# Optimization experiments

Hardware: AMD Instinct MI355X
Metric: run time of the kernel (lower is better)

## Reference

```python
import jax, jax.numpy as jnp
import numpy as np
import math

T, B, D, H, L, C = 2048, 64, 256, 256, 2, 2
HIGHWAY_BIAS = 0.0
# SRU rescale factor for the highway skip term (rescale=True)
SCALE_X = (1.0 + math.exp(HIGHWAY_BIAS * 2)) ** 0.5


def setup_inputs() -> dict:
    key = jax.random.key(0)
    ks = jax.random.split(key, 8)
    s = 1.0 / np.sqrt(D)
    x = jax.random.normal(ks[0], (T, B, D), dtype=jnp.float32)
    # per-layer SRU weights: W [D, 3H] -> (x_tilde, f, r); bias [2H] -> (b_f, b_r)
    W1 = jax.random.uniform(ks[1], (D, 3 * H), jnp.float32, -s, s)
    b1 = jnp.zeros((2 * H,), jnp.float32)
    W2 = jax.random.uniform(ks[2], (H, 3 * H), jnp.float32, -s, s)
    b2 = jnp.zeros((2 * H,), jnp.float32)
    lin_W = jax.random.uniform(ks[3], (H, C), jnp.float32, -s, s)
    lin_b = jnp.zeros((C,), jnp.float32)
    return {"x": x, "W1": W1, "b1": b1, "W2": W2, "b2": b2,
            "lin_W": lin_W, "lin_b": lin_b}


def _sru_layer(x, W, b):
    # x: [T, B, D]; W: [D, 3H]; b: [2H]. Skip term uses raw x (D == H).
    U = jnp.einsum('tbd,dk->tbk', x, W)           # [T, B, 3H]
    x_tilde, f_raw, r_raw = jnp.split(U, 3, axis=-1)
    b_f, b_r = jnp.split(b, 2)
    f = jax.nn.sigmoid(f_raw + b_f + HIGHWAY_BIAS)  # [T, B, H]
    r = jax.nn.sigmoid(r_raw + b_r)                 # [T, B, H]

    def step(c, inp):
        f_t, xt_t = inp
        c = f_t * c + (1.0 - f_t) * xt_t
        return c, c

    c0 = jnp.zeros(x.shape[1:], x.dtype)            # [B, H]
    _, cs = jax.lax.scan(step, c0, (f, x_tilde))    # cs: [T, B, H]
    h = r * cs + (1.0 - r) * (x * SCALE_X)          # highway skip (rescaled)
    return h


def reference(x, W1, b1, W2, b2, lin_W, lin_b):
    h1 = _sru_layer(x, W1, b1)
    h2 = _sru_layer(h1, W2, b2)
    last = h2[-1]                                   # [B, H] (last timestep)
    # Dropout in eval mode = identity (deterministic reference)
    return last @ lin_W + lin_b                     # [B, C]
```

## Files before the change

kernel.cpp:

```cpp
#include <hip/hip_runtime.h>
#include <hip/hip_bf16.h>
#include <stdint.h>

#define T_LEN 2048
#define B_SZ  64
#define H_SZ  256
#define NH3   768
#define M_SZ  (T_LEN * B_SZ)
#define NC    64
#define TC    32
#define SCALE_X_F 1.41421356237309515f

typedef __attribute__((ext_vector_type(8))) short short8;
typedef __attribute__((ext_vector_type(4))) float f32x4;

__device__ __forceinline__ float sigmoidf_(float z) {
    return 1.0f / (1.0f + __expf(-z));
}
__device__ __forceinline__ unsigned short f2bf(float f) {
    unsigned u = __float_as_uint(f);
    return (unsigned short)((u + 0x7FFFu + ((u >> 16) & 1u)) >> 16);
}
__device__ __forceinline__ float bf2f(unsigned short s) {
    return __uint_as_float(((unsigned)s) << 16);
}

__global__ void k_convert_x(const float* __restrict__ x, unsigned short* __restrict__ xb) {
    int i = blockIdx.x * blockDim.x + threadIdx.x;
    const float4* in = (const float4*)x;
    float4 a = in[i * 2];
    float4 b = in[i * 2 + 1];
    short8 o;
    o[0] = (short)f2bf(a.x); o[1] = (short)f2bf(a.y);
    o[2] = (short)f2bf(a.z); o[3] = (short)f2bf(a.w);
    o[4] = (short)f2bf(b.x); o[5] = (short)f2bf(b.y);
    o[6] = (short)f2bf(b.z); o[7] = (short)f2bf(b.w);
    *(short8*)&xb[(size_t)i * 8] = o;
}

__global__ void k_prep_w(const float* __restrict__ W, unsigned short* __restrict__ Wt) {
    int i = blockIdx.x * 256 + threadIdx.x;
    int n = i >> 8, k = i & 255;
    Wt[i] = f2bf(W[(size_t)k * NH3 + n]);
}

template <int NT, int CS>
__global__ void k_gemm(const unsigned short* __restrict__ A,
                       const unsigned short* __restrict__ Bt,
                       unsigned short* __restrict__ C) {
    __shared__ alignas(16) unsigned short smem[128 * 128];
    unsigned short* As = smem;
    unsigned short* Bs = smem + 8192;

    const int cpx = (1024 * NT) / 8;
    int orig = blockIdx.x;
    int wgid = (orig & 7) * cpx + (orig >> 3);
    int mt = wgid / NT, nt = wgid % NT;
    int mbase = mt * 128, nbase = nt * 128;

    int tid = threadIdx.x;
    int w = tid >> 6, l = tid & 63;
    int r16 = l & 15, kg = l >> 4;
    int wr = w >> 1, wc = w & 1;
    int scol = ((l & 7) ^ (l >> 3)) * 8;
    int srow = (l >> 3);

    f32x4 acc[4][4];
    #pragma unroll
    for (int m = 0; m < 4; ++m)
        #pragma unroll
        for (int n = 0; n < 4; ++n) {
            f32x4 z = {0.f, 0.f, 0.f, 0.f};
            acc[m][n] = z;
        }

    for (int kt = 0; kt < 4; ++kt) {
        int k0 = kt * 64;
        #pragma unroll
        for (int p = 0; p < 4; ++p) {
            int row = w * 32 + p * 8 + srow;
            const unsigned short* ga = A  + (size_t)(mbase + row) * 256 + k0 + scol;
            const unsigned short* gb = Bt + (size_t)(nbase + row) * 256 + k0 + scol;
            __builtin_amdgcn_global_load_lds(
                (const __attribute__((address_space(1))) void*)ga,
                (__attribute__((address_space(3))) void*)&As[(w * 4 + p) * 512], 16, 0, 0);
            __builtin_amdgcn_global_load_lds(
                (const __attribute__((address_space(1))) void*)gb,
                (__attribute__((address_space(3))) void*)&Bs[(w * 4 + p) * 512], 16, 0, 0);
        }
        __syncthreads();

        short8 af[4][2], bfv[4][2];
        #pragma unroll
        for (int m = 0; m < 4; ++m) {
            int arow = wr * 64 + m * 16 + r16;
            int sw = (arow & 7) << 3;
            #pragma unroll
            for (int kk = 0; kk < 2; ++kk)
                af[m][kk] = *(const short8*)&As[arow * 64 + ((kk * 32 + kg * 8) ^ sw)];
        }
        #pragma unroll
        for (int n = 0; n < 4; ++n) {
            int brow = wc * 64 + n * 16 + r16;
            int sw = (brow & 7) << 3;
            #pragma unroll
            for (int kk = 0; kk < 2; ++kk)
                bfv[n][kk] = *(const short8*)&Bs[brow * 64 + ((kk * 32 + kg * 8) ^ sw)];
        }

        #pragma unroll
        for (int m = 0; m < 4; ++m)
            #pragma unroll
            for (int n = 0; n < 4; ++n)
                #pragma unroll
                for (int kk = 0; kk < 2; ++kk)
                    acc[m][n] = __builtin_amdgcn_mfma_f32_16x16x32_bf16(
                        af[m][kk], bfv[n][kk], acc[m][n], 0, 0, 0);
        __syncthreads();
    }

    #pragma unroll
    for (int m = 0; m < 4; ++m)
        #pragma unroll
        for (int n = 0; n < 4; ++n) {
            int col = wc * 64 + n * 16 + r16;
            #pragma unroll
            for (int r = 0; r < 4; ++r) {
                int row = wr * 64 + m * 16 + kg * 4 + r;
                smem[row * 128 + (col ^ ((row & 7) << 3))] = f2bf(acc[m][n][r]);
            }
        }
    __syncthreads();
    #pragma unroll
    for (int i = 0; i < 8; ++i) {
        int slot = i * 256 + tid;
        int row = slot >> 4, seg = slot & 15;
        short8 v = *(const short8*)&smem[row * 128 + ((seg * 8) ^ ((row & 7) << 3))];
        *(short8*)&C[(size_t)(mbase + row) * CS + nbase + seg * 8] = v;
    }
}

__global__ void k_passA(const unsigned short* __restrict__ U, const float* __restrict__ bias,
                        float* __restrict__ P, float* __restrict__ S, int stride) {
    int ci = blockIdx.x >> 6;
    int b  = blockIdx.x & 63;
    int h  = threadIdx.x;
    float bfv = bias[h];
    size_t base = ((size_t)(ci * TC) * B_SZ + b) * stride + h;
    float c = 0.f, pr = 1.f;
    #pragma unroll 4
    for (int t = 0; t < TC; ++t) {
        float xt = bf2f(U[base]);
        float fr = bf2f(U[base + 256]);
        float f = sigmoidf_(fr + bfv);
        c = f * c + (1.f - f) * xt;
        pr *= f;
        base += (size_t)B_SZ * stride;
    }
    int o = blockIdx.x * 256 + h;
    P[o] = pr;
    S[o] = c;
}

__global__ void k_passB(const float* __restrict__ P, const float* __restrict__ S,
                        float* __restrict__ cin) {
    int b = blockIdx.x, h = threadIdx.x;
    int idx = b * 256 + h;
    float c = 0.f;
    #pragma unroll 8
    for (int ci = 0; ci < NC; ++ci) {
        cin[ci * 16384 + idx] = c;
        c = P[ci * 16384 + idx] * c + S[ci * 16384 + idx];
    }
    cin[NC * 16384 + idx] = c;
}

__global__ void k_passC(const unsigned short* __restrict__ U, const float* __restrict__ bias,
                        const unsigned short* __restrict__ xb, const float* __restrict__ cin,
                        unsigned short* __restrict__ hout) {
    int ci = blockIdx.x >> 6, b = blockIdx.x & 63, h = threadIdx.x;
    float bfv = bias[h], brv = bias[256 + h];
    float c = cin[blockIdx.x * 256 + h];
    size_t base  = ((size_t)(ci * TC) * B_SZ + b) * NH3 + h;
    size_t xbase = ((size_t)(ci * TC) * B_SZ + b) * H_SZ + h;
    #pragma unroll 4
    for (int t = 0; t < TC; ++t) {
        float xt = bf2f(U[base]);
        float fr = bf2f(U[base + 256]);
        float rr = bf2f(U[base + 512]);
        float f = sigmoidf_(fr + bfv);
        float r = sigmoidf_(rr + brv);
        c = f * c + (1.f - f) * xt;
        float xv = bf2f(xb[xbase]);
        hout[xbase] = f2bf(r * c + (1.f - r) * xv * SCALE_X_F);
        base  += (size_t)B_SZ * NH3;
        xbase += (size_t)B_SZ * H_SZ;
    }
}

__global__ void k_final(const unsigned short* __restrict__ h1, const float* __restrict__ cin,
                        const float* __restrict__ W2, const float* __restrict__ b2,
                        const float* __restrict__ lw, const float* __restrict__ lb,
                        float* __restrict__ out) {
    int b = blockIdx.x, h = threadIdx.x;
    __shared__ float hrow[256];
    size_t hb = ((size_t)(T_LEN - 1) * B_SZ + b) * H_SZ;
    hrow[h] = bf2f(h1[hb + h]);
    __syncthreads();
    float rr = 0.f;
    #pragma unroll 8
    for (int k = 0; k < 256; ++k)
        rr += hrow[k] * W2[(size_t)k * NH3 + 512 + h];
    float r = sigmoidf_(rr + b2[256 + h]);
    float c = cin[NC * 16384 + b * 256 + h];
    float hv = r * c + (1.f - r) * hrow[h] * SCALE_X_F;
    float p0 = hv * lw[h * 2];
    float p1 = hv * lw[h * 2 + 1];
    #pragma unroll
    for (int off = 32; off; off >>= 1) {
        p0 += __shfl_down(p0, off);
        p1 += __shfl_down(p1, off);
    }
    __shared__ float s0[4], s1[4];
    int wid = h >> 6, lane = h & 63;
    if (lane == 0) { s0[wid] = p0; s1[wid] = p1; }
    __syncthreads();
    if (h == 0) {
        out[b * 2]     = s0[0] + s0[1] + s0[2] + s0[3] + lb[0];
        out[b * 2 + 1] = s1[0] + s1[1] + s1[2] + s1[3] + lb[1];
    }
}

extern "C" void kernel_launch(void* const* d_in, const int* in_sizes, int n_in,
                              void* d_out, int out_size, void* d_ws, size_t ws_size,
                              hipStream_t stream) {
    const float* x   = (const float*)d_in[0];
    const float* W1  = (const float*)d_in[1];
    const float* b1  = (const float*)d_in[2];
    const float* W2  = (const float*)d_in[3];
    const float* b2  = (const float*)d_in[4];
    const float* lw  = (const float*)d_in[5];
    const float* lb  = (const float*)d_in[6];
    float* out = (float*)d_out;

    char* ws = (char*)d_ws;
    unsigned short* U   = (unsigned short*)ws;
    unsigned short* xb  = (unsigned short*)(ws + 201326592);
    unsigned short* h1  = (unsigned short*)(ws + 268435456);
    unsigned short* Wt1 = (unsigned short*)(ws + 335544320);
    unsigned short* Wt2 = (unsigned short*)(ws + 335937536);
    float* Pbuf = (float*)(ws + 336330752);
    float* Sbuf = (float*)(ws + 340525056);
    float* cin  = (float*)(ws + 344719360);

    k_convert_x<<<16384, 256, 0, stream>>>(x, xb);
    k_prep_w<<<768, 256, 0, stream>>>(W1, Wt1);
    k_prep_w<<<512, 256, 0, stream>>>(W2, Wt2);

    k_gemm<6, NH3><<<6144, 256, 0, stream>>>(xb, Wt1, U);
    k_passA<<<4096, 256, 0, stream>>>(U, b1, Pbuf, Sbuf, NH3);
    k_passB<<<64, 256, 0, stream>>>(Pbuf, Sbuf, cin);
    k_passC<<<4096, 256, 0, stream>>>(U, b1, xb, cin, h1);

    k_gemm<4, 512><<<4096, 256, 0, stream>>>(h1, Wt2, U);
    k_passA<<<4096, 256, 0, stream>>>(U, b2, Pbuf, Sbuf, 512);
    k_passB<<<64, 256, 0, stream>>>(Pbuf, Sbuf, cin);
    k_final<<<64, 256, 0, stream>>>(h1, cin, W2, b2, lw, lb, out);
}
```

Baseline: 413.6 us.

## Double-buffer LDS tiles in bf16 GEMM to overlap loads with MFMA

The projection GEMM now keeps two LDS buffers each for the A and B tiles. It issues the global-to-LDS loads for the next K-slice before running the MFMAs on the current one, and drops one barrier per iteration. The goal is to hide global memory latency behind matrix compute. In exchange, LDS use per block doubles and a launch bound of 2 blocks per CU is added, which may reduce occupancy.

```diff
diff --git a/kernel.cpp b/kernel.cpp
--- a/kernel.cpp
+++ b/kernel.cpp
@@ -45,12 +45,12 @@
 }
 
 template <int NT, int CS>
-__global__ void k_gemm(const unsigned short* __restrict__ A,
-                       const unsigned short* __restrict__ Bt,
-                       unsigned short* __restrict__ C) {
-    __shared__ alignas(16) unsigned short smem[128 * 128];
-    unsigned short* As = smem;
-    unsigned short* Bs = smem + 8192;
+__global__ void __launch_bounds__(256, 2)
+k_gemm(const unsigned short* __restrict__ A,
+       const unsigned short* __restrict__ Bt,
+       unsigned short* __restrict__ C) {
+    __shared__ alignas(16) unsigned short As[2][8192];
+    __shared__ alignas(16) unsigned short Bs[2][8192];
 
     const int cpx = (1024 * NT) / 8;
     int orig = blockIdx.x;
@@ -65,6 +65,22 @@
     int scol = ((l & 7) ^ (l >> 3)) * 8;
     int srow = (l >> 3);
 
+    const unsigned short* aBase = A  + (size_t)(mbase + w * 32 + srow) * 256 + scol;
+    const unsigned short* bBase = Bt + (size_t)(nbase + w * 32 + srow) * 256 + scol;
+
+    #define STAGE(buf, kt)                                                        \
+        do {                                                                      \
+            _Pragma("unroll")                                                     \
+            for (int p = 0; p < 4; ++p) {                                         \
+                __builtin_amdgcn_global_load_lds(                                 \
+                    (const __attribute__((address_space(1))) void*)(aBase + (size_t)p * 8 * 256 + (kt) * 64), \
+                    (__attribute__((address_space(3))) void*)&As[buf][(w * 4 + p) * 512], 16, 0, 0); \
+                __builtin_amdgcn_global_load_lds(                                 \
+                    (const __attribute__((address_space(1))) void*)(bBase + (size_t)p * 8 * 256 + (kt) * 64), \
+                    (__attribute__((address_space(3))) void*)&Bs[buf][(w * 4 + p) * 512], 16, 0, 0); \
+            }                                                                     \
+        } while (0)
+
     f32x4 acc[4][4];
     #pragma unroll
     for (int m = 0; m < 4; ++m)
@@ -74,21 +90,13 @@
             acc[m][n] = z;
         }
 
+    STAGE(0, 0);
+    __syncthreads();
+
+    int cur = 0;
+    #pragma unroll
     for (int kt = 0; kt < 4; ++kt) {
-        int k0 = kt * 64;
-        #pragma unroll
-        for (int p = 0; p < 4; ++p) {
-            int row = w * 32 + p * 8 + srow;
-            const unsigned short* ga = A  + (size_t)(mbase + row) * 256 + k0 + scol;
-            const unsigned short* gb = Bt + (size_t)(nbase + row) * 256 + k0 + scol;
-            __builtin_amdgcn_global_load_lds(
-                (const __attribute__((address_space(1))) void*)ga,
-                (__attribute__((address_space(3))) void*)&As[(w * 4 + p) * 512], 16, 0, 0);
-            __builtin_amdgcn_global_load_lds(
-                (const __attribute__((address_space(1))) void*)gb,
-                (__attribute__((address_space(3))) void*)&Bs[(w * 4 + p) * 512], 16, 0, 0);
-        }
-        __syncthreads();
+        if (kt < 3) STAGE(cur ^ 1, kt + 1);
 
         short8 af[4][2], bfv[4][2];
         #pragma unroll
@@ -97,7 +105,7 @@
             int sw = (arow & 7) << 3;
             #pragma unroll
             for (int kk = 0; kk < 2; ++kk)
-                af[m][kk] = *(const short8*)&As[arow * 64 + ((kk * 32 + kg * 8) ^ sw)];
+                af[m][kk] = *(const short8*)&As[cur][arow * 64 + ((kk * 32 + kg * 8) ^ sw)];
         }
         #pragma unroll
         for (int n = 0; n < 4; ++n) {
@@ -105,7 +113,7 @@
             int sw = (brow & 7) << 3;
             #pragma unroll
             for (int kk = 0; kk < 2; ++kk)
-                bfv[n][kk] = *(const short8*)&Bs[brow * 64 + ((kk * 32 + kg * 8) ^ sw)];
+                bfv[n][kk] = *(const short8*)&Bs[cur][brow * 64 + ((kk * 32 + kg * 8) ^ sw)];
         }
 
         #pragma unroll
@@ -116,9 +124,13 @@
                 for (int kk = 0; kk < 2; ++kk)
                     acc[m][n] = __builtin_amdgcn_mfma_f32_16x16x32_bf16(
                         af[m][kk], bfv[n][kk], acc[m][n], 0, 0, 0);
+
         __syncthreads();
-    }
-
+        cur ^= 1;
+    }
+    #undef STAGE
+
+    unsigned short* smem = &As[0][0];
     #pragma unroll
     for (int m = 0; m < 4; ++m)
         #pragma unroll
```

After: 389.2 us. -5.9%, faster.

## Load GEMM MFMA fragments directly from global memory, dropping LDS staging

Applied to the files above, without the earlier changes.

The GEMM kernel no longer stages A and B tiles through LDS with global_load_lds and barriers. Each lane now reads its MFMA operand fragments straight from global memory over a fully unrolled K loop, and __launch_bounds__(256,4) is added to raise occupancy. This removes the LDS round trip and the per-step __syncthreads, but gives up reuse of loaded tiles across waves, so global and L2 traffic and load latency increase.

```diff
diff --git a/kernel.cpp b/kernel.cpp
--- a/kernel.cpp
+++ b/kernel.cpp
@@ -45,12 +45,11 @@
 }
 
 template <int NT, int CS>
-__global__ void k_gemm(const unsigned short* __restrict__ A,
-                       const unsigned short* __restrict__ Bt,
-                       unsigned short* __restrict__ C) {
+__global__ void __launch_bounds__(256, 4)
+k_gemm(const unsigned short* __restrict__ A,
+       const unsigned short* __restrict__ Bt,
+       unsigned short* __restrict__ C) {
     __shared__ alignas(16) unsigned short smem[128 * 128];
-    unsigned short* As = smem;
-    unsigned short* Bs = smem + 8192;
 
     const int cpx = (1024 * NT) / 8;
     int orig = blockIdx.x;
@@ -62,8 +61,15 @@
     int w = tid >> 6, l = tid & 63;
     int r16 = l & 15, kg = l >> 4;
     int wr = w >> 1, wc = w & 1;
-    int scol = ((l & 7) ^ (l >> 3)) * 8;
-    int srow = (l >> 3);
+
+    const unsigned short* ap[4];
+    const unsigned short* bp[4];
+    #pragma unroll
+    for (int m = 0; m < 4; ++m)
+        ap[m] = A + (size_t)(mbase + wr * 64 + m * 16 + r16) * 256 + kg * 8;
+    #pragma unroll
+    for (int n = 0; n < 4; ++n)
+        bp[n] = Bt + (size_t)(nbase + wc * 64 + n * 16 + r16) * 256 + kg * 8;
 
     f32x4 acc[4][4];
     #pragma unroll
@@ -74,49 +80,21 @@
             acc[m][n] = z;
         }
 
-    for (int kt = 0; kt < 4; ++kt) {
-        int k0 = kt * 64;
-        #pragma unroll
-        for (int p = 0; p < 4; ++p) {
-            int row = w * 32 + p * 8 + srow;
-            const unsigned short* ga = A  + (size_t)(mbase + row) * 256 + k0 + scol;
-            const unsigned short* gb = Bt + (size_t)(nbase + row) * 256 + k0 + scol;
-            __builtin_amdgcn_global_load_lds(
-                (const __attribute__((address_space(1))) void*)ga,
-                (__attribute__((address_space(3))) void*)&As[(w * 4 + p) * 512], 16, 0, 0);
-            __builtin_amdgcn_global_load_lds(
-                (const __attribute__((address_space(1))) void*)gb,
-                (__attribute__((address_space(3))) void*)&Bs[(w * 4 + p) * 512], 16, 0, 0);
-        }
-        __syncthreads();
-
-        short8 af[4][2], bfv[4][2];
-        #pragma unroll
-        for (int m = 0; m < 4; ++m) {
-            int arow = wr * 64 + m * 16 + r16;
-            int sw = (arow & 7) << 3;
-            #pragma unroll
-            for (int kk = 0; kk < 2; ++kk)
-                af[m][kk] = *(const short8*)&As[arow * 64 + ((kk * 32 + kg * 8) ^ sw)];
-        }
-        #pragma unroll
-        for (int n = 0; n < 4; ++n) {
-            int brow = wc * 64 + n * 16 + r16;
-            int sw = (brow & 7) << 3;
-            #pragma unroll
-            for (int kk = 0; kk < 2; ++kk)
-                bfv[n][kk] = *(const short8*)&Bs[brow * 64 + ((kk * 32 + kg * 8) ^ sw)];
-        }
-
+    #pragma unroll
+    for (int kt = 0; kt < 8; ++kt) {
+        short8 af[4], bfv[4];
+        #pragma unroll
+        for (int m = 0; m < 4; ++m)
+            af[m] = *(const short8*)(ap[m] + kt * 32);
+        #pragma unroll
+        for (int n = 0; n < 4; ++n)
+            bfv[n] = *(const short8*)(bp[n] + kt * 32);
         #pragma unroll
         for (int m = 0; m < 4; ++m)
             #pragma unroll
             for (int n = 0; n < 4; ++n)
-                #pragma unroll
-                for (int kk = 0; kk < 2; ++kk)
-                    acc[m][n] = __builtin_amdgcn_mfma_f32_16x16x32_bf16(
-                        af[m][kk], bfv[n][kk], acc[m][n], 0, 0, 0);
-        __syncthreads();
+                acc[m][n] = __builtin_amdgcn_mfma_f32_16x16x32_bf16(
+                    af[m], bfv[n], acc[m][n], 0, 0, 0);
     }
 
     #pragma unroll
```

Result: slower. 516.7 us (+24.9%).

## Make GEMM persistent with double-buffered LDS prefetch across K-steps and tiles

Applied to the files above, without the earlier changes.

Turns the bf16 MFMA GEMM into a persistent kernel that launches 512 blocks, each processing a contiguous run of 12 or 8 output tiles. Global-to-LDS loads for the next K-step, or the first K-step of the next tile, are issued into a second LDS buffer before the current step computes, so load latency overlaps with MFMA work. It also raises wave priority around the MFMA block and sets launch bounds for two blocks per CU. The cost is doubled LDS use, which may limit occupancy, and a more fragile manual waitcnt and barrier schedule.

```diff
diff --git a/kernel.cpp b/kernel.cpp
--- a/kernel.cpp
+++ b/kernel.cpp
@@ -44,19 +44,16 @@
     Wt[i] = f2bf(W[(size_t)k * NH3 + n]);
 }
 
-template <int NT, int CS>
-__global__ void k_gemm(const unsigned short* __restrict__ A,
-                       const unsigned short* __restrict__ Bt,
-                       unsigned short* __restrict__ C) {
-    __shared__ alignas(16) unsigned short smem[128 * 128];
-    unsigned short* As = smem;
-    unsigned short* Bs = smem + 8192;
-
-    const int cpx = (1024 * NT) / 8;
+template <int NT, int CS, int TPB>
+__global__ void __launch_bounds__(256, 2)
+k_gemm(const unsigned short* __restrict__ A,
+       const unsigned short* __restrict__ Bt,
+       unsigned short* __restrict__ C) {
+    __shared__ alignas(16) unsigned short lds[2][16384];
+
     int orig = blockIdx.x;
-    int wgid = (orig & 7) * cpx + (orig >> 3);
-    int mt = wgid / NT, nt = wgid % NT;
-    int mbase = mt * 128, nbase = nt * 128;
+    int wgid = (orig & 7) * 64 + (orig >> 3);
+    int t0 = wgid * TPB;
 
     int tid = threadIdx.x;
     int w = tid >> 6, l = tid & 63;
@@ -65,78 +62,108 @@
     int scol = ((l & 7) ^ (l >> 3)) * 8;
     int srow = (l >> 3);
 
-    f32x4 acc[4][4];
-    #pragma unroll
-    for (int m = 0; m < 4; ++m)
-        #pragma unroll
-        for (int n = 0; n < 4; ++n) {
-            f32x4 z = {0.f, 0.f, 0.f, 0.f};
-            acc[m][n] = z;
-        }
-
-    for (int kt = 0; kt < 4; ++kt) {
-        int k0 = kt * 64;
+    auto stage = [&](int t, int kt, int b) {
+        int mb = (t / NT) * 128, nb = (t % NT) * 128;
         #pragma unroll
         for (int p = 0; p < 4; ++p) {
             int row = w * 32 + p * 8 + srow;
-            const unsigned short* ga = A  + (size_t)(mbase + row) * 256 + k0 + scol;
-            const unsigned short* gb = Bt + (size_t)(nbase + row) * 256 + k0 + scol;
+            const unsigned short* ga = A  + (size_t)(mb + row) * 256 + kt * 64 + scol;
+            const unsigned short* gb = Bt + (size_t)(nb + row) * 256 + kt * 64 + scol;
             __builtin_amdgcn_global_load_lds(
                 (const __attribute__((address_space(1))) void*)ga,
-                (__attribute__((address_space(3))) void*)&As[(w * 4 + p) * 512], 16, 0, 0);
+                (__attribute__((address_space(3))) void*)&lds[b][(w * 4 + p) * 512], 16, 0, 0);
             __builtin_amdgcn_global_load_lds(
                 (const __attribute__((address_space(1))) void*)gb,
-                (__attribute__((address_space(3))) void*)&Bs[(w * 4 + p) * 512], 16, 0, 0);
+                (__attribute__((address_space(3))) void*)&lds[b][8192 + (w * 4 + p) * 512], 16, 0, 0);
         }
-        __syncthreads();
-
-        short8 af[4][2], bfv[4][2];
-        #pragma unroll
-        for (int m = 0; m < 4; ++m) {
-            int arow = wr * 64 + m * 16 + r16;
-            int sw = (arow & 7) << 3;
-            #pragma unroll
-            for (int kk = 0; kk < 2; ++kk)
-                af[m][kk] = *(const short8*)&As[arow * 64 + ((kk * 32 + kg * 8) ^ sw)];
+    };
+
+    stage(t0, 0, 0);
+
+    #pragma unroll 1
+    for (int i = 0; i < TPB; ++i) {
+        int t = t0 + i;
+
+        f32x4 acc[4][4];
+        #pragma unroll
+        for (int m = 0; m < 4; ++m)
+            #pragma unroll
+            for (int n = 0; n < 4; ++n) {
+                f32x4 z = {0.f, 0.f, 0.f, 0.f};
+                acc[m][n] = z;
+            }
+
+        #pragma unroll
+        for (int kt = 0; kt < 4; ++kt) {
+            if (kt < 3) stage(t, kt + 1, (kt + 1) & 1);
+            else        stage(min(t + 1, t0 + TPB - 1), 0, 0);
+
+            asm volatile("s_waitcnt vmcnt(8)" ::: "memory");
+            __builtin_amdgcn_s_barrier();
+            asm volatile("" ::: "memory");
+
+            const unsigned short* As = &lds[kt & 1][0];
+            const unsigned short* Bs = &lds[kt & 1][8192];
+            short8 af[4][2], bfv[4][2];
+            #pragma unroll
+            for (int m = 0; m < 4; ++m) {
+                int arow = wr * 64 + m * 16 + r16;
+                int sw = (arow & 7) << 3;
+                #pragma unroll
+                for (int kk = 0; kk < 2; ++kk)
+                    af[m][kk] = *(const short8*)&As[arow * 64 + ((kk * 32 + kg * 8) ^ sw)];
+            }
+            #pragma unroll
+            for (int n = 0; n < 4; ++n) {
+                int brow = wc * 64 + n * 16 + r16;
+                int sw = (brow & 7) << 3;
+                #pragma unroll
+                for (int kk = 0; kk < 2; ++kk)
+                    bfv[n][kk] = *(const short8*)&Bs[brow * 64 + ((kk * 32 + kg * 8) ^ sw)];
+            }
+
+            __builtin_amdgcn_s_setprio(1);
+            #pragma unroll
+            for (int m = 0; m < 4; ++m)
+                #pragma unroll
+                for (int n = 0; n < 4; ++n)
+                    #pragma unroll
+                    for (int kk = 0; kk < 2; ++kk)
+                        acc[m][n] = __builtin_amdgcn_mfma_f32_16x16x32_bf16(
+                            af[m][kk], bfv[n][kk], acc[m][n], 0, 0, 0);
+            __builtin_amdgcn_s_setprio(0);
+
+            asm volatile("" ::: "memory");
+            __builtin_amdgcn_s_barrier();
+            asm volatile("" ::: "memory");
         }
-        #pragma unroll
-        for (int n = 0; n < 4; ++n) {
-            int brow = wc * 64 + n * 16 + r16;
-            int sw = (brow & 7) << 3;
-            #pragma unroll
-            for (int kk = 0; kk < 2; ++kk)
-                bfv[n][kk] = *(const short8*)&Bs[brow * 64 + ((kk * 32 + kg * 8) ^ sw)];
+
+        unsigned short* ep = &lds[1][0];
+        int mbase = (t / NT) * 128, nbase = (t % NT) * 128;
+        #pragma unroll
+        for (int m = 0; m < 4; ++m)
+            #pragma unroll
+            for (int n = 0; n < 4; ++n) {
+                int col = wc * 64 + n * 16 + r16;
+                #pragma unroll
+                for (int r = 0; r < 4; ++r) {
+                    int row = wr * 64 + m * 16 + kg * 4 + r;
+                    ep[row * 128 + (col ^ ((row & 7) << 3))] = f2bf(acc[m][n][r]);
+                }
+            }
+        asm volatile("s_waitcnt lgkmcnt(0)" ::: "memory");
+        __builtin_amdgcn_s_barrier();
+        asm volatile("" ::: "memory");
+        #pragma unroll
+        for (int s = 0; s < 8; ++s) {
+            int slot = s * 256 + tid;
+            int row = slot >> 4, seg = slot & 15;
+            short8 v = *(const short8*)&ep[row * 128 + ((seg * 8) ^ ((row & 7) << 3))];
+            *(short8*)&C[(size_t)(mbase + row) * CS + nbase + seg * 8] = v;
         }
-
-        #pragma unroll
-        for (int m = 0; m < 4; ++m)
-            #pragma unroll
-            for (int n = 0; n < 4; ++n)
-                #pragma unroll
-                for (int kk = 0; kk < 2; ++kk)
-                    acc[m][n] = __builtin_amdgcn_mfma_f32_16x16x32_bf16(
-                        af[m][kk], bfv[n][kk], acc[m][n], 0, 0, 0);
-        __syncthreads();
-    }
-
-    #pragma unroll
-    for (int m = 0; m < 4; ++m)
-        #pragma unroll
-        for (int n = 0; n < 4; ++n) {
-            int col = wc * 64 + n * 16 + r16;
-            #pragma unroll
-            for (int r = 0; r < 4; ++r) {
-                int row = wr * 64 + m * 16 + kg * 4 + r;
-                smem[row * 128 + (col ^ ((row & 7) << 3))] = f2bf(acc[m][n][r]);
-            }
-        }
-    __syncthreads();
-    #pragma unroll
-    for (int i = 0; i < 8; ++i) {
-        int slot = i * 256 + tid;
-        int row = slot >> 4, seg = slot & 15;
-        short8 v = *(const short8*)&smem[row * 128 + ((seg * 8) ^ ((row & 7) << 3))];
-        *(short8*)&C[(size_t)(mbase + row) * CS + nbase + seg * 8] = v;
+        asm volatile("s_waitcnt lgkmcnt(0)" ::: "memory");
+        __builtin_amdgcn_s_barrier();
+        asm volatile("" ::: "memory");
     }
 }
 
@@ -257,12 +284,12 @@
     k_prep_w<<<768, 256, 0, stream>>>(W1, Wt1);
     k_prep_w<<<512, 256, 0, stream>>>(W2, Wt2);
 
-    k_gemm<6, NH3><<<6144, 256, 0, stream>>>(xb, Wt1, U);
+    k_gemm<6, NH3, 12><<<512, 256, 0, stream>>>(xb, Wt1, U);
     k_passA<<<4096, 256, 0, stream>>>(U, b1, Pbuf, Sbuf, NH3);
     k_passB<<<64, 256, 0, stream>>>(Pbuf, Sbuf, cin);
     k_passC<<<4096, 256, 0, stream>>>(U, b1, xb, cin, h1);
 
-    k_gemm<4, 512><<<4096, 256, 0, stream>>>(h1, Wt2, U);
+    k_gemm<4, 512, 8><<<512, 256, 0, stream>>>(h1, Wt2, U);
     k_passA<<<4096, 256, 0, stream>>>(U, b2, Pbuf, Sbuf, 512);
     k_passB<<<64, 256, 0, stream>>>(Pbuf, Sbuf, cin);
     k_final<<<64, 256, 0, stream>>>(h1, cin, W2, b2, lw, lb, out);
```

Result: faster. 347.4 us (-16.0%).
